# Kernel tuning notes

Hardware: AMD Instinct MI355X
Metric: run time of the kernel (lower is better)

Reference implementation:

```python
import jax, jax.numpy as jnp
import numpy as np

B, P, M = 2, 2048, 1024
H, D = 16, 64  # num_heads, head_dim; M == H*D

def setup_inputs() -> dict:
    key = jax.random.key(0)
    k1, k2, k3 = jax.random.split(key, 3)
    x = jax.random.normal(k1, (B, P, M), dtype=jnp.float32)
    W_attn = jax.random.normal(k2, (M, 3 * M), dtype=jnp.float32) * 0.02
    b_attn = jnp.zeros((3 * M,), dtype=jnp.float32)
    W_proj = jax.random.normal(k3, (M, M), dtype=jnp.float32) * 0.02
    b_proj = jnp.zeros((M,), dtype=jnp.float32)
    return {"x": x, "W_attn": W_attn, "b_attn": b_attn, "W_proj": W_proj, "b_proj": b_proj}

def reference(x, W_attn, b_attn, W_proj, b_proj):
    b, p, m = x.shape
    # fused QKV projection
    qkv = jnp.einsum('bpm,mn->bpn', x, W_attn) + b_attn  # [b,p,3m]
    q, k, v = jnp.split(qkv, 3, axis=2)
    q = q.reshape(b, p, H, D)
    k = k.reshape(b, p, H, D)
    v = v.reshape(b, p, H, D)
    q = q / jnp.sqrt(jnp.asarray(D, dtype=q.dtype))
    scores = jnp.einsum('bqhd,bkhd->bhqk', q, k)  # [b,h,p,p]
    causal = jnp.tril(jnp.ones((p, p), dtype=bool))  # [p,p]
    big_neg = jnp.finfo(jnp.float32).min
    scores = jnp.where(causal[None, None, :, :], scores, big_neg)
    pattern = jax.nn.softmax(scores, axis=-1)
    z = jnp.einsum('bhqk,bkhd->bqhd', pattern, v)  # [b,p,h,d]
    z = z.reshape(b, p, m)
    out = jnp.einsum('bpm,mn->bpn', z, W_proj) + b_proj
    return out
```

## Files before the change

### kernel.cpp

```cpp
#include <hip/hip_runtime.h>
#include <hip/hip_bf16.h>

typedef __bf16 bf16;
typedef __attribute__((ext_vector_type(8))) __bf16 bf16x8;
typedef __attribute__((ext_vector_type(4))) float f32x4;

#define MFMA16(a, b, c) __builtin_amdgcn_mfma_f32_16x16x32_bf16(a, b, c, 0, 0, 0)
#define GLL16(gp, lp)                                                          \
  __builtin_amdgcn_global_load_lds(                                            \
      (const __attribute__((address_space(1))) void*)(gp),                     \
      (__attribute__((address_space(3))) void*)(lp), 16, 0, 0)

constexpr int Bsz = 2, Pseq = 2048, Mdim = 1024, NH = 16, Dh = 64;
constexpr int ROWS = Bsz * Pseq;
constexpr float LOG2E = 1.4426950408889634f;
constexpr float BIG_NEG = -3.0e38f;
constexpr float M0 = 8.0f;

__global__ __launch_bounds__(256) void k_pre(const float* __restrict__ X,
                                             bf16* __restrict__ Xb,
                                             const float* __restrict__ Wa,
                                             bf16* __restrict__ Wat,
                                             const float* __restrict__ Wp,
                                             bf16* __restrict__ Wpt) {
  __shared__ __align__(16) bf16 tile[64][72];
  int blk = blockIdx.x;
  int t = threadIdx.x;
  if (blk < 1024) {
    const f32x4* X4 = (const f32x4*)X;
    int i0 = blk * 1024 + t;
#pragma unroll
    for (int c = 0; c < 4; ++c) {
      int i = i0 + c * 256;
      f32x4 v = X4[i];
      union { bf16 h[4]; uint2 u; } pk;
      pk.h[0] = (bf16)v[0]; pk.h[1] = (bf16)v[1];
      pk.h[2] = (bf16)v[2]; pk.h[3] = (bf16)v[3];
      ((uint2*)Xb)[i] = pk.u;
    }
    return;
  }
  const float* W; bf16* Wt; int Ndim, n0, k0;
  if (blk < 1792) {
    int bx = blk - 1024;
    W = Wa; Wt = Wat; Ndim = 3 * Mdim;
    n0 = (bx % 48) * 64; k0 = (bx / 48) * 64;
  } else {
    int bx = blk - 1792;
    W = Wp; Wt = Wpt; Ndim = Mdim;
    n0 = (bx & 15) * 64; k0 = (bx >> 4) * 64;
  }
  int tc = t & 15, tr = t >> 4;
#pragma unroll
  for (int pass = 0; pass < 4; ++pass) {
    int r = tr + pass * 16;
    f32x4 v = *(const f32x4*)(W + (size_t)(k0 + r) * Ndim + n0 + tc * 4);
#pragma unroll
    for (int i = 0; i < 4; ++i) tile[tc * 4 + i][r] = (bf16)v[i];
  }
  __syncthreads();
#pragma unroll
  for (int pass = 0; pass < 4; ++pass) {
    int n = tr + pass * 16;
    union { bf16 h[4]; uint2 u; } pk;
#pragma unroll
    for (int i = 0; i < 4; ++i) pk.h[i] = tile[n][tc * 4 + i];
    *(uint2*)(Wt + (size_t)(n0 + n) * Mdim + k0 + tc * 4) = pk.u;
  }
}

template <int TM, int TN>
__device__ __forceinline__ void gemm_core(const bf16* __restrict__ A,
                                          const bf16* __restrict__ Bt,
                                          bf16* Ash, bf16* Bsh, int K,
                                          int row0, int col0,
                                          f32x4 (&acc)[TM / 32][TN / 32]) {
  constexpr int MT = TM / 32, NT = TN / 32;
  int tid = threadIdx.x;
  int lane = tid & 63, w = tid >> 6;
  int l15 = lane & 15, g = lane >> 4, l7 = lane & 7, l8 = lane >> 3;
  int wm = w & 1, wn = w >> 1;
  const bf16* Ag = A + (size_t)(row0 + w * 8 + l8) * K + (l7 ^ l8) * 8;
  const bf16* Bg = Bt + (size_t)(col0 + w * 8 + l8) * K + (l7 ^ l8) * 8;
  bf16* Asb = Ash + w * 512;
  bf16* Bsb = Bsh + w * 512;
  for (int k0 = 0; k0 < K; k0 += 64) {
#pragma unroll
    for (int p = 0; p < MT; ++p)
      GLL16(Ag + (size_t)(p * 32) * K + k0, Asb + p * 2048);
#pragma unroll
    for (int p = 0; p < NT; ++p)
      GLL16(Bg + (size_t)(p * 32) * K + k0, Bsb + p * 2048);
    __syncthreads();
#pragma unroll
    for (int ks = 0; ks < 2; ++ks) {
      int swz = ((ks * 4 + g) ^ l7) * 8;
      bf16x8 af[MT], bfr[NT];
#pragma unroll
      for (int mt = 0; mt < MT; ++mt)
        af[mt] = *(const bf16x8*)(Ash + (wm * (TM / 2) + mt * 16 + l15) * 64 + swz);
#pragma unroll
      for (int nt = 0; nt < NT; ++nt)
        bfr[nt] = *(const bf16x8*)(Bsh + (wn * (TN / 2) + nt * 16 + l15) * 64 + swz);
#pragma unroll
      for (int mt = 0; mt < MT; ++mt)
#pragma unroll
        for (int nt = 0; nt < NT; ++nt)
          acc[mt][nt] = MFMA16(af[mt], bfr[nt], acc[mt][nt]);
    }
    __syncthreads();
  }
}

__global__ __launch_bounds__(512) void k_qkv(const bf16* __restrict__ Xb,
                                             const bf16* __restrict__ Wt,
                                             const float* __restrict__ bias,
                                             bf16* __restrict__ Qo,
                                             bf16* __restrict__ Ko,
                                             bf16* __restrict__ Vto) {
  __shared__ __align__(16) bf16 Ash[128 * 64], Bsh[128 * 64];
  int cb = blockIdx.x, rb = blockIdx.y;
  int row0 = rb * 128, col0 = cb * 128;
  int tid = threadIdx.x;
  int lane = tid & 63, w = tid >> 6;
  int l15 = lane & 15, g = lane >> 4, l7 = lane & 7;
  int wm = w & 1, wn = w >> 1;
  int sr = tid >> 3;
  int sc = (tid & 7) ^ (sr & 7);
  const bf16* Ag = Xb + (size_t)(row0 + sr) * Mdim + sc * 8;
  const bf16* Bg = Wt + (size_t)(col0 + sr) * Mdim + sc * 8;

  f32x4 acc[4][2];
  const f32x4 zero = {0.f, 0.f, 0.f, 0.f};
#pragma unroll
  for (int mt = 0; mt < 4; ++mt)
#pragma unroll
    for (int nt = 0; nt < 2; ++nt) acc[mt][nt] = zero;

  for (int k0 = 0; k0 < Mdim; k0 += 64) {
    GLL16(Ag + k0, Ash + tid * 8);
    GLL16(Ag + (size_t)64 * Mdim + k0, Ash + 4096 + tid * 8);
    GLL16(Bg + k0, Bsh + tid * 8);
    GLL16(Bg + (size_t)64 * Mdim + k0, Bsh + 4096 + tid * 8);
    __syncthreads();
#pragma unroll
    for (int ks = 0; ks < 2; ++ks) {
      int swz = ((ks * 4 + g) ^ l7) * 8;
      bf16x8 af[4], bfr[2];
#pragma unroll
      for (int mt = 0; mt < 4; ++mt)
        af[mt] = *(const bf16x8*)(Ash + (wm * 64 + mt * 16 + l15) * 64 + swz);
#pragma unroll
      for (int nt = 0; nt < 2; ++nt)
        bfr[nt] = *(const bf16x8*)(Bsh + (wn * 32 + nt * 16 + l15) * 64 + swz);
#pragma unroll
      for (int mt = 0; mt < 4; ++mt)
#pragma unroll
        for (int nt = 0; nt < 2; ++nt)
          acc[mt][nt] = MFMA16(af[mt], bfr[nt], acc[mt][nt]);
    }
    __syncthreads();
  }

  int sec = cb >> 3;
  if (sec < 2) {
    bf16* out = sec == 0 ? Qo : Ko;
    float scale = sec == 0 ? (0.125f * LOG2E) : 1.0f;
#pragma unroll
    for (int nt = 0; nt < 2; ++nt) {
      int col = col0 + wn * 32 + nt * 16 + l15;
      int cm = col & 1023;
      int h = cm >> 6, d = cm & 63;
      float bv = bias[col];
#pragma unroll
      for (int mt = 0; mt < 4; ++mt)
#pragma unroll
        for (int r = 0; r < 4; ++r) {
          int row = row0 + wm * 64 + mt * 16 + g * 4 + r;
          int b = row >> 11, p = row & 2047;
          out[(size_t)((b * NH + h) * Pseq + p) * Dh + d] =
              (bf16)((acc[mt][nt][r] + bv) * scale);
        }
    }
  } else {
#pragma unroll
    for (int nt = 0; nt < 2; ++nt) {
      int col = col0 + wn * 32 + nt * 16 + l15;
      int cm = col & 1023;
      int h = cm >> 6, d = cm & 63;
      float bv = bias[col];
#pragma unroll
      for (int mt = 0; mt < 4; ++mt) {
        int row = row0 + wm * 64 + mt * 16 + g * 4;
        int b = row >> 11, p = row & 2047;
        union { bf16 hh[4]; uint2 u; } pk;
#pragma unroll
        for (int r = 0; r < 4; ++r) pk.hh[r] = (bf16)(acc[mt][nt][r] + bv);
        *(uint2*)(Vto + ((size_t)((b * NH + h) * Dh + d)) * Pseq + p) = pk.u;
      }
    }
  }
}

__global__ __launch_bounds__(256, 4) void k_attn(const bf16* __restrict__ Q,
                                                 const bf16* __restrict__ K,
                                                 const bf16* __restrict__ Vt,
                                                 bf16* __restrict__ Z) {
  __shared__ __align__(16) bf16 Ksh[2 * 64 * 64];
  __shared__ __align__(16) bf16 Vsh[2 * 64 * 64];
  __shared__ float Lsh[2][32];
  int bh = blockIdx.x;
  int y = blockIdx.y;
  int a = y & 7, bq = y >> 3;
  int qt = (bq == 0) ? a : (bq == 1) ? (15 - a) : (bq == 2) ? (16 + a) : (31 - a);
  int b = bh >> 4, h = bh & 15;
  const bf16* Qb = Q + (size_t)bh * Pseq * Dh;
  const bf16* Kb = K + (size_t)bh * Pseq * Dh;
  const bf16* Vb = Vt + (size_t)bh * Dh * Pseq;
  int tid = threadIdx.x;
  int lane = tid & 63, w = tid >> 6;
  int wq = w & 1, wk = w >> 1;
  int l15 = lane & 15, g = lane >> 4, l7 = lane & 7;
  int q0 = qt * 64;
  int njt = qt + 1;

  bf16x8 qf[2][2];
#pragma unroll
  for (int ks = 0; ks < 2; ++ks)
#pragma unroll
    for (int qg = 0; qg < 2; ++qg)
      qf[ks][qg] = *(const bf16x8*)(Qb + (size_t)(q0 + wq * 32 + qg * 16 + l15) * Dh +
                                    ks * 32 + g * 8);

  f32x4 O[4][2];
  const f32x4 zero = {0.f, 0.f, 0.f, 0.f};
#pragma unroll
  for (int nt = 0; nt < 4; ++nt)
#pragma unroll
    for (int qg = 0; qg < 2; ++qg) O[nt][qg] = zero;
  float lacc[2][4] = {{0.f, 0.f, 0.f, 0.f}, {0.f, 0.f, 0.f, 0.f}};

  int srow = tid >> 3;
  int sgr = (tid & 7) ^ (srow & 7);
  const bf16* Kgs = Kb + (size_t)srow * Dh + sgr * 8;
  const bf16* Vgs = Vb + (size_t)srow * Pseq + sgr * 8;

#pragma unroll
  for (int p = 0; p < 2; ++p) {
    GLL16(Kgs + (size_t)(p * 32) * Dh, Ksh + p * 2048 + tid * 8);
    GLL16(Vgs + (size_t)(p * 32) * Pseq, Vsh + p * 2048 + tid * 8);
  }

  for (int j = 0; j < njt; ++j) {
    int buf = j & 1;
    __syncthreads();
    if (j + 1 < njt) {
      const bf16* Kg2 = Kgs + (size_t)((j + 1) * 64) * Dh;
      const bf16* Vg2 = Vgs + (j + 1) * 64;
      bf16* kd = Ksh + (buf ^ 1) * 4096 + tid * 8;
      bf16* vd = Vsh + (buf ^ 1) * 4096 + tid * 8;
#pragma unroll
      for (int p = 0; p < 2; ++p) {
        GLL16(Kg2 + (size_t)(p * 32) * Dh, kd + p * 2048);
        GLL16(Vg2 + (size_t)(p * 32) * Pseq, vd + p * 2048);
      }
    }
    f32x4 S[2][2];
#pragma unroll
    for (int mtL = 0; mtL < 2; ++mtL)
#pragma unroll
      for (int qg = 0; qg < 2; ++qg) S[mtL][qg] = zero;
    const bf16* Kr = Ksh + buf * 4096;
    const bf16* Vr = Vsh + buf * 4096;
    __builtin_amdgcn_s_setprio(1);
#pragma unroll
    for (int ks = 0; ks < 2; ++ks) {
      int swz = ((ks * 4 + g) ^ l7) * 8;
#pragma unroll
      for (int mtL = 0; mtL < 2; ++mtL) {
        bf16x8 kf = *(const bf16x8*)(Kr + (wk * 32 + mtL * 16 + l15) * 64 + swz);
        S[mtL][0] = MFMA16(kf, qf[ks][0], S[mtL][0]);
        S[mtL][1] = MFMA16(kf, qf[ks][1], S[mtL][1]);
      }
    }
    __builtin_amdgcn_s_setprio(0);
    if (j == njt - 1) {
#pragma unroll
      for (int qg = 0; qg < 2; ++qg) {
        int q = q0 + wq * 32 + qg * 16 + l15;
#pragma unroll
        for (int mtL = 0; mtL < 2; ++mtL) {
          int kvb = j * 64 + wk * 32 + mtL * 16 + g * 4;
#pragma unroll
          for (int r = 0; r < 4; ++r)
            if (kvb + r > q) S[mtL][qg][r] = BIG_NEG;
        }
      }
    }
    bf16x8 pf[2];
#pragma unroll
    for (int qg = 0; qg < 2; ++qg) {
      unsigned wv[2][2];
#pragma unroll
      for (int mtL = 0; mtL < 2; ++mtL) {
        float p0 = __builtin_amdgcn_exp2f(S[mtL][qg][0] - M0);
        float p1 = __builtin_amdgcn_exp2f(S[mtL][qg][1] - M0);
        float p2 = __builtin_amdgcn_exp2f(S[mtL][qg][2] - M0);
        float p3 = __builtin_amdgcn_exp2f(S[mtL][qg][3] - M0);
        lacc[qg][0] += p0; lacc[qg][1] += p1;
        lacc[qg][2] += p2; lacc[qg][3] += p3;
        asm("v_cvt_pk_bf16_f32 %0, %1, %2" : "=v"(wv[mtL][0]) : "v"(p0), "v"(p1));
        asm("v_cvt_pk_bf16_f32 %0, %1, %2" : "=v"(wv[mtL][1]) : "v"(p2), "v"(p3));
      }
#pragma unroll
      for (int s = 0; s < 2; ++s) {
        asm("v_permlane32_swap_b32 %0, %1" : "+v"(wv[0][s]), "+v"(wv[1][s]));
        asm("v_permlane16_swap_b32 %0, %1" : "+v"(wv[0][s]), "+v"(wv[1][s]));
      }
      union { unsigned u[4]; bf16x8 v; } pa;
      pa.u[0] = wv[0][0]; pa.u[1] = wv[0][1];
      pa.u[2] = wv[1][0]; pa.u[3] = wv[1][1];
      pf[qg] = pa.v;
    }
    __builtin_amdgcn_s_setprio(1);
    {
      int swzv = ((wk * 4 + g) ^ l7) * 8;
#pragma unroll
      for (int nt = 0; nt < 4; ++nt) {
        bf16x8 vf = *(const bf16x8*)(Vr + (nt * 16 + l15) * 64 + swzv);
        O[nt][0] = MFMA16(pf[0], vf, O[nt][0]);
        O[nt][1] = MFMA16(pf[1], vf, O[nt][1]);
      }
    }
    __builtin_amdgcn_s_setprio(0);
  }
  float lh[2];
#pragma unroll
  for (int qg = 0; qg < 2; ++qg) {
    float l = (lacc[qg][0] + lacc[qg][1]) + (lacc[qg][2] + lacc[qg][3]);
    l += __shfl_xor(l, 16);
    l += __shfl_xor(l, 32);
    lh[qg] = l;
  }
  int fb = ((njt - 1) & 1) ^ 1;
  float* Osh = (float*)((wq ? Vsh : Ksh) + fb * 4096);
  if (wk) {
#pragma unroll
    for (int qg = 0; qg < 2; ++qg) {
#pragma unroll
      for (int nt = 0; nt < 4; ++nt)
#pragma unroll
        for (int r = 0; r < 4; ++r)
          Osh[(qg * 16 + g * 4 + r) * 64 + nt * 16 + l15] = O[nt][qg][r];
      if (g == 0) Lsh[wq][qg * 16 + l15] = lh[qg];
    }
  }
  __syncthreads();
  if (!wk) {
#pragma unroll
    for (int qg = 0; qg < 2; ++qg) {
      float lt = lh[qg] + Lsh[wq][qg * 16 + l15];
#pragma unroll
      for (int r = 0; r < 4; ++r) {
        float li = __shfl(lt, g * 4 + r);
        float inv = 1.0f / li;
        int q = q0 + wq * 32 + qg * 16 + g * 4 + r;
        size_t base = ((size_t)(b * Pseq + q)) * Mdim + h * Dh;
#pragma unroll
        for (int nt = 0; nt < 4; ++nt) {
          float val = O[nt][qg][r] + Osh[(qg * 16 + g * 4 + r) * 64 + nt * 16 + l15];
          Z[base + nt * 16 + l15] = (bf16)(val * inv);
        }
      }
    }
  }
}

__global__ __launch_bounds__(256) void k_proj(const bf16* __restrict__ Zb,
                                              const bf16* __restrict__ Wt,
                                              const float* __restrict__ bias,
                                              float* __restrict__ Out) {
  __shared__ __align__(16) bf16 Ash[128 * 64], Bsh[64 * 64];
  int cb = blockIdx.x, rb = blockIdx.y;
  int row0 = rb * 128, col0 = cb * 64;
  f32x4 acc[4][2];
  const f32x4 zero = {0.f, 0.f, 0.f, 0.f};
#pragma unroll
  for (int mt = 0; mt < 4; ++mt)
#pragma unroll
    for (int nt = 0; nt < 2; ++nt) acc[mt][nt] = zero;
  gemm_core<128, 64>(Zb, Wt, Ash, Bsh, Mdim, row0, col0, acc);

  int lane = threadIdx.x & 63, w = threadIdx.x >> 6;
  int l15 = lane & 15, g = lane >> 4;
  int wm = w & 1, wn = w >> 1;
#pragma unroll
  for (int nt = 0; nt < 2; ++nt) {
    int col = col0 + wn * 32 + nt * 16 + l15;
    float bv = bias[col];
#pragma unroll
    for (int mt = 0; mt < 4; ++mt)
#pragma unroll
      for (int r = 0; r < 4; ++r) {
        int row = row0 + wm * 64 + mt * 16 + g * 4 + r;
        Out[(size_t)row * Mdim + col] = acc[mt][nt][r] + bv;
      }
  }
}

extern "C" void kernel_launch(void* const* d_in, const int* in_sizes, int n_in,
                              void* d_out, int out_size, void* d_ws, size_t ws_size,
                              hipStream_t stream) {
  const float* x = (const float*)d_in[0];
  const float* W_attn = (const float*)d_in[1];
  const float* b_attn = (const float*)d_in[2];
  const float* W_proj = (const float*)d_in[3];
  const float* b_proj = (const float*)d_in[4];
  float* out = (float*)d_out;

  bf16* Xb = (bf16*)d_ws;
  bf16* Wat = Xb + (size_t)ROWS * Mdim;
  bf16* Wpt = Wat + (size_t)3 * Mdim * Mdim;
  bf16* Qs = Wpt + (size_t)Mdim * Mdim;
  bf16* Ks = Qs + (size_t)ROWS * Mdim;
  bf16* Vts = Ks + (size_t)ROWS * Mdim;
  bf16* Zb = Vts + (size_t)ROWS * Mdim;

  k_pre<<<2048, 256, 0, stream>>>(x, Xb, W_attn, Wat, W_proj, Wpt);
  k_qkv<<<dim3(3 * Mdim / 128, ROWS / 128), 512, 0, stream>>>(Xb, Wat, b_attn, Qs, Ks, Vts);
  k_attn<<<dim3(Bsz * NH, 32), 256, 0, stream>>>(Qs, Ks, Vts, Zb);
  k_proj<<<dim3(Mdim / 64, ROWS / 128), 256, 0, stream>>>(Zb, Wpt, b_proj, out);
}
```

Before: 169.4 us.

## Load K/V MFMA fragments directly from global memory, dropping LDS staging

The attention kernel stops staging K and V tiles through double-buffered shared memory with global_load_lds and per-iteration barriers. Each wave now loads its own K and V MFMA fragments straight from global memory into registers. Shared memory is kept only for the final cross-wave reduction of O. This removes the barriers and the LDS traffic, at the cost of loads that are no longer prefetched one tile ahead, duplicate global reads across waves (each K fragment is loaded by both wq waves, and every wave loads all four V fragments), and more exposed memory latency.

```diff
diff --git a/kernel.cpp b/kernel.cpp
--- a/kernel.cpp
+++ b/kernel.cpp
@@ -206,8 +206,7 @@
                                                  const bf16* __restrict__ K,
                                                  const bf16* __restrict__ Vt,
                                                  bf16* __restrict__ Z) {
-  __shared__ __align__(16) bf16 Ksh[2 * 64 * 64];
-  __shared__ __align__(16) bf16 Vsh[2 * 64 * 64];
+  __shared__ __align__(16) float Osh[2][32 * 64];
   __shared__ float Lsh[2][32];
   int bh = blockIdx.x;
   int y = blockIdx.y;
@@ -220,7 +219,7 @@
   int tid = threadIdx.x;
   int lane = tid & 63, w = tid >> 6;
   int wq = w & 1, wk = w >> 1;
-  int l15 = lane & 15, g = lane >> 4, l7 = lane & 7;
+  int l15 = lane & 15, g = lane >> 4;
   int q0 = qt * 64;
   int njt = qt + 1;
 
@@ -240,49 +239,35 @@
     for (int qg = 0; qg < 2; ++qg) O[nt][qg] = zero;
   float lacc[2][4] = {{0.f, 0.f, 0.f, 0.f}, {0.f, 0.f, 0.f, 0.f}};
 
-  int srow = tid >> 3;
-  int sgr = (tid & 7) ^ (srow & 7);
-  const bf16* Kgs = Kb + (size_t)srow * Dh + sgr * 8;
-  const bf16* Vgs = Vb + (size_t)srow * Pseq + sgr * 8;
-
-#pragma unroll
-  for (int p = 0; p < 2; ++p) {
-    GLL16(Kgs + (size_t)(p * 32) * Dh, Ksh + p * 2048 + tid * 8);
-    GLL16(Vgs + (size_t)(p * 32) * Pseq, Vsh + p * 2048 + tid * 8);
-  }
+  const bf16* Kp = Kb + (size_t)(wk * 32 + l15) * Dh + g * 8;
+  const bf16* Vp = Vb + (size_t)l15 * Pseq + wk * 32 + g * 8;
 
   for (int j = 0; j < njt; ++j) {
-    int buf = j & 1;
-    __syncthreads();
-    if (j + 1 < njt) {
-      const bf16* Kg2 = Kgs + (size_t)((j + 1) * 64) * Dh;
-      const bf16* Vg2 = Vgs + (j + 1) * 64;
-      bf16* kd = Ksh + (buf ^ 1) * 4096 + tid * 8;
-      bf16* vd = Vsh + (buf ^ 1) * 4096 + tid * 8;
-#pragma unroll
-      for (int p = 0; p < 2; ++p) {
-        GLL16(Kg2 + (size_t)(p * 32) * Dh, kd + p * 2048);
-        GLL16(Vg2 + (size_t)(p * 32) * Pseq, vd + p * 2048);
-      }
-    }
+    bf16x8 kf00 = *(const bf16x8*)(Kp);
+    bf16x8 kf01 = *(const bf16x8*)(Kp + 1024);
+    bf16x8 kf10 = *(const bf16x8*)(Kp + 32);
+    bf16x8 kf11 = *(const bf16x8*)(Kp + 1024 + 32);
+    bf16x8 vf0 = *(const bf16x8*)(Vp);
+    bf16x8 vf1 = *(const bf16x8*)(Vp + (size_t)16 * Pseq);
+    bf16x8 vf2 = *(const bf16x8*)(Vp + (size_t)32 * Pseq);
+    bf16x8 vf3 = *(const bf16x8*)(Vp + (size_t)48 * Pseq);
+    Kp += 4096;
+    Vp += 64;
+
     f32x4 S[2][2];
 #pragma unroll
     for (int mtL = 0; mtL < 2; ++mtL)
 #pragma unroll
       for (int qg = 0; qg < 2; ++qg) S[mtL][qg] = zero;
-    const bf16* Kr = Ksh + buf * 4096;
-    const bf16* Vr = Vsh + buf * 4096;
     __builtin_amdgcn_s_setprio(1);
-#pragma unroll
-    for (int ks = 0; ks < 2; ++ks) {
-      int swz = ((ks * 4 + g) ^ l7) * 8;
-#pragma unroll
-      for (int mtL = 0; mtL < 2; ++mtL) {
-        bf16x8 kf = *(const bf16x8*)(Kr + (wk * 32 + mtL * 16 + l15) * 64 + swz);
-        S[mtL][0] = MFMA16(kf, qf[ks][0], S[mtL][0]);
-        S[mtL][1] = MFMA16(kf, qf[ks][1], S[mtL][1]);
-      }
-    }
+    S[0][0] = MFMA16(kf00, qf[0][0], S[0][0]);
+    S[0][1] = MFMA16(kf00, qf[0][1], S[0][1]);
+    S[1][0] = MFMA16(kf01, qf[0][0], S[1][0]);
+    S[1][1] = MFMA16(kf01, qf[0][1], S[1][1]);
+    S[0][0] = MFMA16(kf10, qf[1][0], S[0][0]);
+    S[0][1] = MFMA16(kf10, qf[1][1], S[0][1]);
+    S[1][0] = MFMA16(kf11, qf[1][0], S[1][0]);
+    S[1][1] = MFMA16(kf11, qf[1][1], S[1][1]);
     __builtin_amdgcn_s_setprio(0);
     if (j == njt - 1) {
 #pragma unroll
@@ -323,15 +308,14 @@
       pf[qg] = pa.v;
     }
     __builtin_amdgcn_s_setprio(1);
-    {
-      int swzv = ((wk * 4 + g) ^ l7) * 8;
-#pragma unroll
-      for (int nt = 0; nt < 4; ++nt) {
-        bf16x8 vf = *(const bf16x8*)(Vr + (nt * 16 + l15) * 64 + swzv);
-        O[nt][0] = MFMA16(pf[0], vf, O[nt][0]);
-        O[nt][1] = MFMA16(pf[1], vf, O[nt][1]);
-      }
-    }
+    O[0][0] = MFMA16(pf[0], vf0, O[0][0]);
+    O[0][1] = MFMA16(pf[1], vf0, O[0][1]);
+    O[1][0] = MFMA16(pf[0], vf1, O[1][0]);
+    O[1][1] = MFMA16(pf[1], vf1, O[1][1]);
+    O[2][0] = MFMA16(pf[0], vf2, O[2][0]);
+    O[2][1] = MFMA16(pf[1], vf2, O[2][1]);
+    O[3][0] = MFMA16(pf[0], vf3, O[3][0]);
+    O[3][1] = MFMA16(pf[1], vf3, O[3][1]);
     __builtin_amdgcn_s_setprio(0);
   }
   float lh[2];
@@ -342,8 +326,6 @@
     l += __shfl_xor(l, 32);
     lh[qg] = l;
   }
-  int fb = ((njt - 1) & 1) ^ 1;
-  float* Osh = (float*)((wq ? Vsh : Ksh) + fb * 4096);
   if (wk) {
 #pragma unroll
     for (int qg = 0; qg < 2; ++qg) {
@@ -351,7 +333,7 @@
       for (int nt = 0; nt < 4; ++nt)
 #pragma unroll
         for (int r = 0; r < 4; ++r)
-          Osh[(qg * 16 + g * 4 + r) * 64 + nt * 16 + l15] = O[nt][qg][r];
+          Osh[wq][(qg * 16 + g * 4 + r) * 64 + nt * 16 + l15] = O[nt][qg][r];
       if (g == 0) Lsh[wq][qg * 16 + l15] = lh[qg];
     }
   }
@@ -368,7 +350,7 @@
         size_t base = ((size_t)(b * Pseq + q)) * Mdim + h * Dh;
 #pragma unroll
         for (int nt = 0; nt < 4; ++nt) {
-          float val = O[nt][qg][r] + Osh[(qg * 16 + g * 4 + r) * 64 + nt * 16 + l15];
+          float val = O[nt][qg][r] + Osh[wq][(qg * 16 + g * 4 + r) * 64 + nt * 16 + l15];
           Z[base + nt * 16 + l15] = (bf16)(val * inv);
         }
       }
```

After: 198.2 us. 17.0% more time.

## Pair complementary 32-row query tiles per attention block for causal balance

Applied to the files above, without the earlier changes.

Each attention block now handles two 32-row query tiles, t and 63-t, one after the other, instead of a single 64-row tile. This makes the number of causal KV tiles the same for every block and removes the tail imbalance of the earlier tile ordering. In exchange, each wave now applies every KV tile to 16 query rows instead of 32, so K/V reuse per load is halved and total K/V loads roughly double. The change also cuts per-wave registers for the O and S accumulators.

```diff
diff --git a/kernel.cpp b/kernel.cpp
--- a/kernel.cpp
+++ b/kernel.cpp
@@ -208,11 +208,9 @@
                                                  bf16* __restrict__ Z) {
   __shared__ __align__(16) bf16 Ksh[2 * 64 * 64];
   __shared__ __align__(16) bf16 Vsh[2 * 64 * 64];
-  __shared__ float Lsh[2][32];
+  __shared__ float Lsh[2][16];
   int bh = blockIdx.x;
-  int y = blockIdx.y;
-  int a = y & 7, bq = y >> 3;
-  int qt = (bq == 0) ? a : (bq == 1) ? (15 - a) : (bq == 2) ? (16 + a) : (31 - a);
+  int pr = blockIdx.y;
   int b = bh >> 4, h = bh & 15;
   const bf16* Qb = Q + (size_t)bh * Pseq * Dh;
   const bf16* Kb = K + (size_t)bh * Pseq * Dh;
@@ -221,94 +219,84 @@
   int lane = tid & 63, w = tid >> 6;
   int wq = w & 1, wk = w >> 1;
   int l15 = lane & 15, g = lane >> 4, l7 = lane & 7;
-  int q0 = qt * 64;
-  int njt = qt + 1;
-
-  bf16x8 qf[2][2];
-#pragma unroll
-  for (int ks = 0; ks < 2; ++ks)
-#pragma unroll
-    for (int qg = 0; qg < 2; ++qg)
-      qf[ks][qg] = *(const bf16x8*)(Qb + (size_t)(q0 + wq * 32 + qg * 16 + l15) * Dh +
-                                    ks * 32 + g * 8);
-
-  f32x4 O[4][2];
-  const f32x4 zero = {0.f, 0.f, 0.f, 0.f};
-#pragma unroll
-  for (int nt = 0; nt < 4; ++nt)
-#pragma unroll
-    for (int qg = 0; qg < 2; ++qg) O[nt][qg] = zero;
-  float lacc[2][4] = {{0.f, 0.f, 0.f, 0.f}, {0.f, 0.f, 0.f, 0.f}};
 
   int srow = tid >> 3;
   int sgr = (tid & 7) ^ (srow & 7);
   const bf16* Kgs = Kb + (size_t)srow * Dh + sgr * 8;
   const bf16* Vgs = Vb + (size_t)srow * Pseq + sgr * 8;
 
-#pragma unroll
-  for (int p = 0; p < 2; ++p) {
-    GLL16(Kgs + (size_t)(p * 32) * Dh, Ksh + p * 2048 + tid * 8);
-    GLL16(Vgs + (size_t)(p * 32) * Pseq, Vsh + p * 2048 + tid * 8);
-  }
-
-  for (int j = 0; j < njt; ++j) {
-    int buf = j & 1;
-    __syncthreads();
-    if (j + 1 < njt) {
-      const bf16* Kg2 = Kgs + (size_t)((j + 1) * 64) * Dh;
-      const bf16* Vg2 = Vgs + (j + 1) * 64;
-      bf16* kd = Ksh + (buf ^ 1) * 4096 + tid * 8;
-      bf16* vd = Vsh + (buf ^ 1) * 4096 + tid * 8;
-#pragma unroll
-      for (int p = 0; p < 2; ++p) {
-        GLL16(Kg2 + (size_t)(p * 32) * Dh, kd + p * 2048);
-        GLL16(Vg2 + (size_t)(p * 32) * Pseq, vd + p * 2048);
-      }
-    }
-    f32x4 S[2][2];
-#pragma unroll
-    for (int mtL = 0; mtL < 2; ++mtL)
-#pragma unroll
-      for (int qg = 0; qg < 2; ++qg) S[mtL][qg] = zero;
-    const bf16* Kr = Ksh + buf * 4096;
-    const bf16* Vr = Vsh + buf * 4096;
-    __builtin_amdgcn_s_setprio(1);
-#pragma unroll
-    for (int ks = 0; ks < 2; ++ks) {
-      int swz = ((ks * 4 + g) ^ l7) * 8;
-#pragma unroll
-      for (int mtL = 0; mtL < 2; ++mtL) {
-        bf16x8 kf = *(const bf16x8*)(Kr + (wk * 32 + mtL * 16 + l15) * 64 + swz);
-        S[mtL][0] = MFMA16(kf, qf[ks][0], S[mtL][0]);
-        S[mtL][1] = MFMA16(kf, qf[ks][1], S[mtL][1]);
-      }
-    }
-    __builtin_amdgcn_s_setprio(0);
-    if (j == njt - 1) {
-#pragma unroll
-      for (int qg = 0; qg < 2; ++qg) {
-        int q = q0 + wq * 32 + qg * 16 + l15;
+  const f32x4 zero = {0.f, 0.f, 0.f, 0.f};
+
+  for (int tt = 0; tt < 2; ++tt) {
+    int t = tt ? 63 - pr : pr;
+    int q0 = t * 32;
+    int njt = t / 2 + 1;
+
+    bf16x8 qf[2];
+#pragma unroll
+    for (int ks = 0; ks < 2; ++ks)
+      qf[ks] = *(const bf16x8*)(Qb + (size_t)(q0 + wq * 16 + l15) * Dh + ks * 32 + g * 8);
+
+    f32x4 O[4];
+#pragma unroll
+    for (int nt = 0; nt < 4; ++nt) O[nt] = zero;
+    float lacc[4] = {0.f, 0.f, 0.f, 0.f};
+
+    __syncthreads();
+#pragma unroll
+    for (int p = 0; p < 2; ++p) {
+      GLL16(Kgs + (size_t)(p * 32) * Dh, Ksh + p * 2048 + tid * 8);
+      GLL16(Vgs + (size_t)(p * 32) * Pseq, Vsh + p * 2048 + tid * 8);
+    }
+
+    for (int j = 0; j < njt; ++j) {
+      int buf = j & 1;
+      __syncthreads();
+      if (j + 1 < njt) {
+        const bf16* Kg2 = Kgs + (size_t)((j + 1) * 64) * Dh;
+        const bf16* Vg2 = Vgs + (j + 1) * 64;
+        bf16* kd = Ksh + (buf ^ 1) * 4096 + tid * 8;
+        bf16* vd = Vsh + (buf ^ 1) * 4096 + tid * 8;
+#pragma unroll
+        for (int p = 0; p < 2; ++p) {
+          GLL16(Kg2 + (size_t)(p * 32) * Dh, kd + p * 2048);
+          GLL16(Vg2 + (size_t)(p * 32) * Pseq, vd + p * 2048);
+        }
+      }
+      f32x4 S[2];
+      S[0] = zero; S[1] = zero;
+      const bf16* Kr = Ksh + buf * 4096;
+      const bf16* Vr = Vsh + buf * 4096;
+      __builtin_amdgcn_s_setprio(1);
+#pragma unroll
+      for (int ks = 0; ks < 2; ++ks) {
+        int swz = ((ks * 4 + g) ^ l7) * 8;
+#pragma unroll
+        for (int mtL = 0; mtL < 2; ++mtL) {
+          bf16x8 kf = *(const bf16x8*)(Kr + (wk * 32 + mtL * 16 + l15) * 64 + swz);
+          S[mtL] = MFMA16(kf, qf[ks], S[mtL]);
+        }
+      }
+      __builtin_amdgcn_s_setprio(0);
+      if (j == njt - 1) {
+        int q = q0 + wq * 16 + l15;
 #pragma unroll
         for (int mtL = 0; mtL < 2; ++mtL) {
           int kvb = j * 64 + wk * 32 + mtL * 16 + g * 4;
 #pragma unroll
           for (int r = 0; r < 4; ++r)
-            if (kvb + r > q) S[mtL][qg][r] = BIG_NEG;
-        }
-      }
-    }
-    bf16x8 pf[2];
-#pragma unroll
-    for (int qg = 0; qg < 2; ++qg) {
+            if (kvb + r > q) S[mtL][r] = BIG_NEG;
+        }
+      }
       unsigned wv[2][2];
 #pragma unroll
       for (int mtL = 0; mtL < 2; ++mtL) {
-        float p0 = __builtin_amdgcn_exp2f(S[mtL][qg][0] - M0);
-        float p1 = __builtin_amdgcn_exp2f(S[mtL][qg][1] - M0);
-        float p2 = __builtin_amdgcn_exp2f(S[mtL][qg][2] - M0);
-        float p3 = __builtin_amdgcn_exp2f(S[mtL][qg][3] - M0);
-        lacc[qg][0] += p0; lacc[qg][1] += p1;
-        lacc[qg][2] += p2; lacc[qg][3] += p3;
+        float p0 = __builtin_amdgcn_exp2f(S[mtL][0] - M0);
+        float p1 = __builtin_amdgcn_exp2f(S[mtL][1] - M0);
+        float p2 = __builtin_amdgcn_exp2f(S[mtL][2] - M0);
+        float p3 = __builtin_amdgcn_exp2f(S[mtL][3] - M0);
+        lacc[0] += p0; lacc[1] += p1;
+        lacc[2] += p2; lacc[3] += p3;
         asm("v_cvt_pk_bf16_f32 %0, %1, %2" : "=v"(wv[mtL][0]) : "v"(p0), "v"(p1));
         asm("v_cvt_pk_bf16_f32 %0, %1, %2" : "=v"(wv[mtL][1]) : "v"(p2), "v"(p3));
       }
@@ -320,55 +308,46 @@
       union { unsigned u[4]; bf16x8 v; } pa;
       pa.u[0] = wv[0][0]; pa.u[1] = wv[0][1];
       pa.u[2] = wv[1][0]; pa.u[3] = wv[1][1];
-      pf[qg] = pa.v;
-    }
-    __builtin_amdgcn_s_setprio(1);
+      __builtin_amdgcn_s_setprio(1);
+      {
+        int swzv = ((wk * 4 + g) ^ l7) * 8;
+#pragma unroll
+        for (int nt = 0; nt < 4; ++nt) {
+          bf16x8 vf = *(const bf16x8*)(Vr + (nt * 16 + l15) * 64 + swzv);
+          O[nt] = MFMA16(pa.v, vf, O[nt]);
+        }
+      }
+      __builtin_amdgcn_s_setprio(0);
+    }
+    float lh;
     {
-      int swzv = ((wk * 4 + g) ^ l7) * 8;
-#pragma unroll
-      for (int nt = 0; nt < 4; ++nt) {
-        bf16x8 vf = *(const bf16x8*)(Vr + (nt * 16 + l15) * 64 + swzv);
-        O[nt][0] = MFMA16(pf[0], vf, O[nt][0]);
-        O[nt][1] = MFMA16(pf[1], vf, O[nt][1]);
-      }
-    }
-    __builtin_amdgcn_s_setprio(0);
-  }
-  float lh[2];
-#pragma unroll
-  for (int qg = 0; qg < 2; ++qg) {
-    float l = (lacc[qg][0] + lacc[qg][1]) + (lacc[qg][2] + lacc[qg][3]);
-    l += __shfl_xor(l, 16);
-    l += __shfl_xor(l, 32);
-    lh[qg] = l;
-  }
-  int fb = ((njt - 1) & 1) ^ 1;
-  float* Osh = (float*)((wq ? Vsh : Ksh) + fb * 4096);
-  if (wk) {
-#pragma unroll
-    for (int qg = 0; qg < 2; ++qg) {
+      float l = (lacc[0] + lacc[1]) + (lacc[2] + lacc[3]);
+      l += __shfl_xor(l, 16);
+      l += __shfl_xor(l, 32);
+      lh = l;
+    }
+    int fb = njt & 1;
+    float* Osh = (float*)((wq ? Vsh : Ksh) + fb * 4096);
+    if (wk) {
 #pragma unroll
       for (int nt = 0; nt < 4; ++nt)
 #pragma unroll
         for (int r = 0; r < 4; ++r)
-          Osh[(qg * 16 + g * 4 + r) * 64 + nt * 16 + l15] = O[nt][qg][r];
-      if (g == 0) Lsh[wq][qg * 16 + l15] = lh[qg];
-    }
-  }
-  __syncthreads();
-  if (!wk) {
-#pragma unroll
-    for (int qg = 0; qg < 2; ++qg) {
-      float lt = lh[qg] + Lsh[wq][qg * 16 + l15];
+          Osh[(g * 4 + r) * 64 + nt * 16 + l15] = O[nt][r];
+      if (g == 0) Lsh[wq][l15] = lh;
+    }
+    __syncthreads();
+    if (!wk) {
+      float lt = lh + Lsh[wq][l15];
 #pragma unroll
       for (int r = 0; r < 4; ++r) {
         float li = __shfl(lt, g * 4 + r);
         float inv = 1.0f / li;
-        int q = q0 + wq * 32 + qg * 16 + g * 4 + r;
+        int q = q0 + wq * 16 + g * 4 + r;
         size_t base = ((size_t)(b * Pseq + q)) * Mdim + h * Dh;
 #pragma unroll
         for (int nt = 0; nt < 4; ++nt) {
-          float val = O[nt][qg][r] + Osh[(qg * 16 + g * 4 + r) * 64 + nt * 16 + l15];
+          float val = O[nt][r] + Osh[(g * 4 + r) * 64 + nt * 16 + l15];
           Z[base + nt * 16 + l15] = (bf16)(val * inv);
         }
       }
```

New measurement: 173.1 us. +2.2%, slower.
